# Kernel tuning notes

Measured on AMD Instinct MI355X. Metric: run time of the kernel, lower is better.

## Reference

```python
import jax, jax.numpy as jnp
import numpy as np

E = 4
K = 2
BN_EPS = 1e-3


def _silu(y):
    return y * jax.nn.sigmoid(y)


def _bn_silu_nchw(y, g, b, m, v):
    # eval-mode BatchNorm2d over channel axis of [B, C, H, W], then SiLU
    scale = (g / jnp.sqrt(v + BN_EPS))[None, :, None, None]
    shift = (b - m * g / jnp.sqrt(v + BN_EPS))[None, :, None, None]
    return _silu(y * scale + shift)


def setup_inputs() -> dict:
    key = jax.random.key(0)
    ks = jax.random.split(key, 20)
    B, C1, C2, H, W = 32, 256, 256, 80, 80
    c_ = C2 // 2  # 128
    s = 0.05
    return {
        "x": jax.random.normal(ks[0], (B, C1, H, W), jnp.float32),
        "w1": jax.random.normal(ks[1], (c_, C1), jnp.float32) * s,
        "bn1_g": jax.random.uniform(ks[2], (c_,), jnp.float32, 0.5, 1.5),
        "bn1_b": jax.random.normal(ks[3], (c_,), jnp.float32) * s,
        "bn1_m": jax.random.normal(ks[4], (c_,), jnp.float32) * s,
        "bn1_v": jax.random.uniform(ks[5], (c_,), jnp.float32, 0.5, 1.5),
        "router_w": jax.random.normal(ks[6], (E, c_), jnp.float32) * s,
        "router_b": jax.random.normal(ks[7], (E,), jnp.float32) * s,
        "ew": jax.random.normal(ks[8], (E, c_, c_, 3, 3), jnp.float32) * s,
        "ebn_g": jax.random.uniform(ks[9], (E, c_), jnp.float32, 0.5, 1.5),
        "ebn_b": jax.random.normal(ks[10], (E, c_), jnp.float32) * s,
        "ebn_m": jax.random.normal(ks[11], (E, c_), jnp.float32) * s,
        "ebn_v": jax.random.uniform(ks[12], (E, c_), jnp.float32, 0.5, 1.5),
        "w3": jax.random.normal(ks[13], (C2, c_), jnp.float32) * s,
        "bn3_g": jax.random.uniform(ks[14], (C2,), jnp.float32, 0.5, 1.5),
        "bn3_b": jax.random.normal(ks[15], (C2,), jnp.float32) * s,
        "bn3_m": jax.random.normal(ks[16], (C2,), jnp.float32) * s,
        "bn3_v": jax.random.uniform(ks[17], (C2,), jnp.float32, 0.5, 1.5),
    }


def reference(x, w1, bn1_g, bn1_b, bn1_m, bn1_v, router_w, router_b,
              ew, ebn_g, ebn_b, ebn_m, ebn_v, w3, bn3_g, bn3_b, bn3_m, bn3_v):
    B, C1, H, W = x.shape
    c_ = w1.shape[0]

    # conv1: 1x1 conv + BN + SiLU -> [B, c_, H, W]
    x_in = _bn_silu_nchw(jnp.einsum('bchw,oc->bohw', x, w1), bn1_g, bn1_b, bn1_m, bn1_v)

    # flatten pixels to tokens [N, c_] (N = B*H*W), matching permute(0,2,3,1).reshape
    tokens = x_in.transpose(0, 2, 3, 1).reshape(-1, c_)
    N = tokens.shape[0]

    # router: 1x1 conv with bias -> per-token logits [N, E]
    logits = tokens @ router_w.T + router_b
    probs = jax.nn.softmax(logits, axis=-1)

    topw, topi = jax.lax.top_k(probs, K)                  # [N, K]
    topw = topw / jnp.sum(topw, axis=-1, keepdims=True)

    # dense [N, E] combine weights: normalized top-k weight where selected, else 0
    wd = jnp.zeros((N, E), tokens.dtype).at[jnp.arange(N)[:, None], topi].set(topw)

    # experts: 3x3 conv applied to 1x1 patches with pad=1 -> only center tap matters
    center = ew[:, :, :, 1, 1]                            # [E, c_out, c_in]
    ye = jnp.einsum('nc,eoc->neo', tokens, center)        # [N, E, c_]
    inv = ebn_g / jnp.sqrt(ebn_v + BN_EPS)                # [E, c_]
    ye = _silu(ye * inv[None] + (ebn_b - ebn_m * inv)[None])

    out_moe = jnp.einsum('neo,ne->no', ye, wd)            # weighted scatter-add
    out_moe = out_moe.reshape(B, H, W, c_).transpose(0, 3, 1, 2)

    # conv3: 1x1 conv + BN + SiLU -> [B, C2, H, W]
    x_out = _bn_silu_nchw(jnp.einsum('bchw,oc->bohw', out_moe, w3), bn3_g, bn3_b, bn3_m, bn3_v)

    # shortcut (c1 == c2 here)
    return x_out + x
```

## Files before the change

kernel.cpp:

```cpp
#include <hip/hip_runtime.h>
#include <cstdint>
#include <cstddef>

#define NEXP 4
#define CH   128
#define C1   256
#define C2   256
#define HWSZ 6400
#define NTOKS 204800
#define BNE  1e-3f

using f32x4 = __attribute__((ext_vector_type(4))) float;
using f16x8 = __attribute__((ext_vector_type(8))) _Float16;
using s16x8 = __attribute__((ext_vector_type(8))) short;

static __device__ __forceinline__ unsigned short f2bf(float f) {
    union { float f; unsigned u; } v; v.f = f;
    unsigned r = v.u + 0x7fffu + ((v.u >> 16) & 1u);
    return (unsigned short)(r >> 16);
}
static __device__ __forceinline__ f32x4 zero4() {
    f32x4 z; z[0] = 0.f; z[1] = 0.f; z[2] = 0.f; z[3] = 0.f; return z;
}
static __device__ __forceinline__ void g2lds16(const void* g, void* l) {
    __builtin_amdgcn_global_load_lds(
        (const __attribute__((address_space(1))) void*)g,
        (__attribute__((address_space(3))) void*)l, 16, 0, 0);
}

#define ASWZ(row) ((((row) >> 1) & 3) << 3)

__global__ __launch_bounds__(256) void k0_pack(const float* __restrict__ ew,
                                               const float* __restrict__ w1,
                                               const float* __restrict__ w3,
                                               unsigned short* __restrict__ cen,
                                               _Float16* __restrict__ w1s,
                                               unsigned short* __restrict__ w3p) {
    int bid = blockIdx.x;
    int tid = threadIdx.x;
    if (bid < 256) {
        int idx = bid * 256 + tid;
        cen[idx] = f2bf(ew[(size_t)idx * 9 + 4]);
    } else if (bid < 384) {
        int lin = (bid - 256) * 256 + tid;
        int o = lin >> 8, k = lin & 255;
        int s = k >> 5, kk = k & 31;
        int kks = kk ^ ASWZ(o);
        float v = w1[o * C1 + k];
        _Float16 h = (_Float16)v;
        w1s[((s * 2 + 0) * 128 + o) * 32 + kks] = h;
        w1s[((s * 2 + 1) * 128 + o) * 32 + kks] = (_Float16)((v - (float)h) * 2048.0f);
    } else {
        int lin = (bid - 384) * 256 + tid;
        int o = lin >> 7, k = lin & 127;
        int s = k >> 5, kk = k & 31;
        int kks = kk ^ ASWZ(o);
        w3p[(s * 256 + o) * 32 + kks] = f2bf(w3[o * CH + k]);
    }
}

__global__ __launch_bounds__(256, 2) void k1_conv1_router(
    const float* __restrict__ x, const _Float16* __restrict__ w1s,
    const float* __restrict__ bn1_g, const float* __restrict__ bn1_b,
    const float* __restrict__ bn1_m, const float* __restrict__ bn1_v,
    const float* __restrict__ rw, const float* __restrict__ rb,
    unsigned short* __restrict__ tokens, float* __restrict__ wd)
{
    const int tid  = threadIdx.x;
    const int lane = tid & 63;
    const int n15  = lane & 15;
    const int quad = lane >> 4;
    const int wv   = tid >> 6;

    const int nt0 = blockIdx.x * 64;
    const int b   = nt0 / HWSZ;
    const int hw0 = nt0 % HWSZ;

    __shared__ union {
        struct { _Float16 Ahl[2 * 128 * 32];
                 _Float16 Bh[64 * 40]; _Float16 Bl[64 * 40]; } s;
        struct { float tok[64 * 132]; float logit[64 * 4]; } e;
    } u;
    __shared__ float s1_l[128], t1_l[128];

    if (tid < 128) {
        float s = bn1_g[tid] / sqrtf(bn1_v[tid] + BNE);
        s1_l[tid] = s;
        t1_l[tid] = bn1_b[tid] - bn1_m[tid] * s;
    }

    f32x4 acc_m[2][4], acc_c[2][4];
    #pragma unroll
    for (int i = 0; i < 2; i++)
        #pragma unroll
        for (int j = 0; j < 4; j++) { acc_m[i][j] = zero4(); acc_c[i][j] = zero4(); }

    const char* w1b = (const char*)w1s;
    char*       Ab  = (char*)u.s.Ahl;

    for (int s = 0; s < 8; s++) {
        {
            const char* src = w1b + s * 16384 + tid * 16;
            char*       dst = Ab + tid * 16;
            g2lds16(src + 0,     dst + 0);
            g2lds16(src + 4096,  dst + 4096);
            g2lds16(src + 8192,  dst + 8192);
            g2lds16(src + 12288, dst + 12288);
        }
        {
            int i  = tid & 63;
            int kg = tid >> 6;
            #pragma unroll
            for (int r = 0; r < 2; r++) {
                int k4 = (kg * 2 + r) * 4;
                const float* xp = x + ((size_t)(b * C1 + s * 32 + k4)) * HWSZ + hw0 + i;
                float v0 = xp[0], v1 = xp[HWSZ], v2 = xp[2 * HWSZ], v3 = xp[3 * HWSZ];
                _Float16* bh = &u.s.Bh[i * 40 + k4];
                _Float16* bl = &u.s.Bl[i * 40 + k4];
                _Float16 h0 = (_Float16)v0, h1 = (_Float16)v1, h2 = (_Float16)v2, h3 = (_Float16)v3;
                bh[0] = h0; bh[1] = h1; bh[2] = h2; bh[3] = h3;
                bl[0] = (_Float16)((v0 - (float)h0) * 2048.0f);
                bl[1] = (_Float16)((v1 - (float)h1) * 2048.0f);
                bl[2] = (_Float16)((v2 - (float)h2) * 2048.0f);
                bl[3] = (_Float16)((v3 - (float)h3) * 2048.0f);
            }
        }
        __syncthreads();

        f16x8 a_h[2], a_l[2];
        #pragma unroll
        for (int mt = 0; mt < 2; mt++) {
            int row = (wv * 2 + mt) * 16 + n15;
            int col = (quad * 8) ^ ASWZ(row);
            a_h[mt] = *(const f16x8*)&u.s.Ahl[row * 32 + col];
            a_l[mt] = *(const f16x8*)&u.s.Ahl[4096 + row * 32 + col];
        }
        #pragma unroll
        for (int nt = 0; nt < 4; nt++) {
            int row = nt * 16 + n15;
            f16x8 b_h = *(const f16x8*)&u.s.Bh[row * 40 + quad * 8];
            f16x8 b_l = *(const f16x8*)&u.s.Bl[row * 40 + quad * 8];
            #pragma unroll
            for (int mt = 0; mt < 2; mt++) {
                acc_m[mt][nt] = __builtin_amdgcn_mfma_f32_16x16x32_f16(a_h[mt], b_h, acc_m[mt][nt], 0, 0, 0);
                acc_c[mt][nt] = __builtin_amdgcn_mfma_f32_16x16x32_f16(a_l[mt], b_h, acc_c[mt][nt], 0, 0, 0);
                acc_c[mt][nt] = __builtin_amdgcn_mfma_f32_16x16x32_f16(a_h[mt], b_l, acc_c[mt][nt], 0, 0, 0);
            }
        }
        __syncthreads();
    }

    #pragma unroll
    for (int mt = 0; mt < 2; mt++)
        #pragma unroll
        for (int nt = 0; nt < 4; nt++)
            #pragma unroll
            for (int r = 0; r < 4; r++) {
                int o  = (wv * 2 + mt) * 16 + quad * 4 + r;
                int tk = nt * 16 + n15;
                float y1 = acc_m[mt][nt][r] + acc_c[mt][nt][r] * (1.0f / 2048.0f);
                float y  = y1 * s1_l[o] + t1_l[o];
                u.e.tok[tk * 132 + o] = y / (1.0f + expf(-y));
            }
    __syncthreads();

    {
        int tk = tid >> 2;
        int e  = tid & 3;
        const float* trow = &u.e.tok[tk * 132];
        const float* wrow = &rw[e * CH];
        float a0 = 0.f, a1 = 0.f, a2 = 0.f, a3 = 0.f;
        #pragma unroll 8
        for (int c = 0; c < CH; c += 4) {
            a0 = fmaf(trow[c + 0], wrow[c + 0], a0);
            a1 = fmaf(trow[c + 1], wrow[c + 1], a1);
            a2 = fmaf(trow[c + 2], wrow[c + 2], a2);
            a3 = fmaf(trow[c + 3], wrow[c + 3], a3);
        }
        u.e.logit[tk * 4 + e] = ((a0 + a1) + (a2 + a3)) + rb[e];
    }
    __syncthreads();

    if (tid < 64) {
        const float* lg = &u.e.logit[tid * 4];
        float l0 = lg[0], l1 = lg[1], l2 = lg[2], l3 = lg[3];
        int i1 = 0; float m1 = l0;
        if (l1 > m1) { m1 = l1; i1 = 1; }
        if (l2 > m1) { m1 = l2; i1 = 2; }
        if (l3 > m1) { m1 = l3; i1 = 3; }
        int i2 = -1; float m2 = -3.4e38f;
        if (i1 != 0 && l0 > m2) { m2 = l0; i2 = 0; }
        if (i1 != 1 && l1 > m2) { m2 = l1; i2 = 1; }
        if (i1 != 2 && l2 > m2) { m2 = l2; i2 = 2; }
        if (i1 != 3 && l3 > m2) { m2 = l3; i2 = 3; }
        float p2 = expf(m2 - m1);
        float wa = 1.0f / (1.0f + p2);
        float wb = p2 * wa;
        float4 wout;
        wout.x = (i1 == 0) ? wa : ((i2 == 0) ? wb : 0.0f);
        wout.y = (i1 == 1) ? wa : ((i2 == 1) ? wb : 0.0f);
        wout.z = (i1 == 2) ? wa : ((i2 == 2) ? wb : 0.0f);
        wout.w = (i1 == 3) ? wa : ((i2 == 3) ? wb : 0.0f);
        *(float4*)&wd[(size_t)(nt0 + tid) * 4] = wout;
    }

    #pragma unroll
    for (int rep = 0; rep < 8; rep++) {
        int lin = rep * 256 + tid;
        int n   = lin >> 5;
        int c4  = (lin & 31) * 4;
        const float* tp = &u.e.tok[n * 132 + c4];
        ushort4 pk;
        pk.x = f2bf(tp[0]); pk.y = f2bf(tp[1]); pk.z = f2bf(tp[2]); pk.w = f2bf(tp[3]);
        *(ushort4*)&tokens[(size_t)(nt0 + n) * CH + c4] = pk;
    }
}

__global__ __launch_bounds__(256, 2) void k2_experts(
    const unsigned short* __restrict__ tokens, const unsigned short* __restrict__ cen,
    const float* __restrict__ wd,
    const float* __restrict__ ebn_g, const float* __restrict__ ebn_b,
    const float* __restrict__ ebn_m, const float* __restrict__ ebn_v,
    unsigned short* __restrict__ moe)
{
    const int tid  = threadIdx.x;
    const int lane = tid & 63;
    const int wv   = tid >> 6;
    const int n15  = lane & 15;
    const int quad = lane >> 4;
    const int qm   = wv & 1;
    const int qn   = wv >> 1;
    const int nt0  = blockIdx.x * 128;

    __shared__ unsigned short Bt[128 * 136];
    __shared__ unsigned short Ac[128 * 136];
    __shared__ float wd_l[512];
    __shared__ float inv_l[512], sh_l[512];

    #pragma unroll
    for (int rep = 0; rep < 8; rep++) {
        int lin = rep * 256 + tid;
        int n   = lin >> 4;
        int c8  = (lin & 15) * 8;
        *(uint4*)&Bt[n * 136 + c8] = *(const uint4*)&tokens[(size_t)(nt0 + n) * CH + c8];
    }
    wd_l[tid]       = wd[(size_t)nt0 * 4 + tid];
    wd_l[256 + tid] = wd[(size_t)nt0 * 4 + 256 + tid];
    #pragma unroll
    for (int r = 0; r < 2; r++) {
        int idx = r * 256 + tid;
        float iv = ebn_g[idx] / sqrtf(ebn_v[idx] + BNE);
        inv_l[idx] = iv;
        sh_l[idx]  = ebn_b[idx] - ebn_m[idx] * iv;
    }

    f32x4 oacc[4][4];
    #pragma unroll
    for (int i = 0; i < 4; i++)
        #pragma unroll
        for (int j = 0; j < 4; j++) oacc[i][j] = zero4();

    for (int e = 0; e < NEXP; e++) {
        __syncthreads();
        #pragma unroll
        for (int rep = 0; rep < 8; rep++) {
            int lin = rep * 256 + tid;
            int o   = lin >> 4;
            int c8  = (lin & 15) * 8;
            *(uint4*)&Ac[o * 136 + c8] = *(const uint4*)&cen[(size_t)e * CH * CH + o * CH + c8];
        }
        __syncthreads();

        f32x4 acc[4][4];
        #pragma unroll
        for (int i = 0; i < 4; i++)
            #pragma unroll
            for (int j = 0; j < 4; j++) acc[i][j] = zero4();

        #pragma unroll
        for (int kk = 0; kk < 4; kk++) {
            int ko = kk * 32 + quad * 8;
            s16x8 a[4], bb[4];
            #pragma unroll
            for (int i = 0; i < 4; i++) {
                a[i]  = *(const s16x8*)&Ac[(qm * 64 + i * 16 + n15) * 136 + ko];
                bb[i] = *(const s16x8*)&Bt[(qn * 64 + i * 16 + n15) * 136 + ko];
            }
            #pragma unroll
            for (int mt = 0; mt < 4; mt++)
                #pragma unroll
                for (int nt = 0; nt < 4; nt++)
                    acc[mt][nt] = __builtin_amdgcn_mfma_f32_16x16x32_bf16(a[mt], bb[nt], acc[mt][nt], 0, 0, 0);
        }

        #pragma unroll
        for (int mt = 0; mt < 4; mt++)
            #pragma unroll
            for (int nt = 0; nt < 4; nt++) {
                float wde = wd_l[(qn * 64 + nt * 16 + n15) * 4 + e];
                #pragma unroll
                for (int r = 0; r < 4; r++) {
                    int o = qm * 64 + mt * 16 + quad * 4 + r;
                    float y = acc[mt][nt][r] * inv_l[e * CH + o] + sh_l[e * CH + o];
                    oacc[mt][nt][r] += wde * (y / (1.0f + __expf(-y)));
                }
            }
    }

    #pragma unroll
    for (int mt = 0; mt < 4; mt++)
        #pragma unroll
        for (int nt = 0; nt < 4; nt++) {
            int tk = qn * 64 + nt * 16 + n15;
            int ob = qm * 64 + mt * 16 + quad * 4;
            ushort4 pk;
            pk.x = f2bf(oacc[mt][nt][0]); pk.y = f2bf(oacc[mt][nt][1]);
            pk.z = f2bf(oacc[mt][nt][2]); pk.w = f2bf(oacc[mt][nt][3]);
            *(ushort4*)&moe[(size_t)(nt0 + tk) * CH + ob] = pk;
        }
}

__global__ __launch_bounds__(256, 2) void k3_conv3(
    const unsigned short* __restrict__ moe, const unsigned short* __restrict__ w3p,
    const float* __restrict__ bn3_g, const float* __restrict__ bn3_b,
    const float* __restrict__ bn3_m, const float* __restrict__ bn3_v,
    const float* __restrict__ x, float* __restrict__ out)
{
    const int tid  = threadIdx.x;
    const int lane = tid & 63;
    const int wv   = tid >> 6;
    const int n15  = lane & 15;
    const int quad = lane >> 4;
    const int nt0  = blockIdx.x * 64;
    const int b    = nt0 / HWSZ;
    const int hw0  = nt0 % HWSZ;

    __shared__ unsigned short A3[256 * 32];
    __shared__ unsigned short B3[64 * 40];
    __shared__ float s3_l[256], t3_l[256];

    {
        float s = bn3_g[tid] / sqrtf(bn3_v[tid] + BNE);
        s3_l[tid] = s;
        t3_l[tid] = bn3_b[tid] - bn3_m[tid] * s;
    }

    f32x4 acc[4][4];
    #pragma unroll
    for (int i = 0; i < 4; i++)
        #pragma unroll
        for (int j = 0; j < 4; j++) acc[i][j] = zero4();

    const char* w3b = (const char*)w3p;
    char*       Ab  = (char*)A3;

    for (int s = 0; s < 4; s++) {
        {
            const char* src = w3b + s * 16384 + tid * 16;
            char*       dst = Ab + tid * 16;
            g2lds16(src + 0,     dst + 0);
            g2lds16(src + 4096,  dst + 4096);
            g2lds16(src + 8192,  dst + 8192);
            g2lds16(src + 12288, dst + 12288);
        }
        #pragma unroll
        for (int rep = 0; rep < 2; rep++) {
            int lin = rep * 256 + tid;
            int n   = lin >> 3;
            int k4  = (lin & 7) * 4;
            *(ushort4*)&B3[n * 40 + k4] = *(const ushort4*)&moe[(size_t)(nt0 + n) * CH + s * 32 + k4];
        }
        __syncthreads();

        s16x8 bf[4];
        #pragma unroll
        for (int nt = 0; nt < 4; nt++)
            bf[nt] = *(const s16x8*)&B3[(nt * 16 + n15) * 40 + quad * 8];
        #pragma unroll
        for (int mt = 0; mt < 4; mt++) {
            int row = (wv * 4 + mt) * 16 + n15;
            int col = (quad * 8) ^ ASWZ(row);
            s16x8 af = *(const s16x8*)&A3[row * 32 + col];
            #pragma unroll
            for (int nt = 0; nt < 4; nt++)
                acc[mt][nt] = __builtin_amdgcn_mfma_f32_16x16x32_bf16(af, bf[nt], acc[mt][nt], 0, 0, 0);
        }
        __syncthreads();
    }

    #pragma unroll
    for (int mt = 0; mt < 4; mt++)
        #pragma unroll
        for (int nt = 0; nt < 4; nt++)
            #pragma unroll
            for (int r = 0; r < 4; r++) {
                int o2 = (wv * 4 + mt) * 16 + quad * 4 + r;
                int tk = nt * 16 + n15;
                size_t g = ((size_t)(b * C2 + o2)) * HWSZ + hw0 + tk;
                float y = acc[mt][nt][r] * s3_l[o2] + t3_l[o2];
                out[g] = y / (1.0f + __expf(-y)) + x[g];
            }
}

extern "C" void kernel_launch(void* const* d_in, const int* in_sizes, int n_in,
                              void* d_out, int out_size, void* d_ws, size_t ws_size,
                              hipStream_t stream) {
    const float* x     = (const float*)d_in[0];
    const float* w1    = (const float*)d_in[1];
    const float* bn1_g = (const float*)d_in[2];
    const float* bn1_b = (const float*)d_in[3];
    const float* bn1_m = (const float*)d_in[4];
    const float* bn1_v = (const float*)d_in[5];
    const float* rw    = (const float*)d_in[6];
    const float* rb    = (const float*)d_in[7];
    const float* ew    = (const float*)d_in[8];
    const float* ebn_g = (const float*)d_in[9];
    const float* ebn_b = (const float*)d_in[10];
    const float* ebn_m = (const float*)d_in[11];
    const float* ebn_v = (const float*)d_in[12];
    const float* w3    = (const float*)d_in[13];
    const float* bn3_g = (const float*)d_in[14];
    const float* bn3_b = (const float*)d_in[15];
    const float* bn3_m = (const float*)d_in[16];
    const float* bn3_v = (const float*)d_in[17];
    float* out = (float*)d_out;

    char* ws = (char*)d_ws;
    unsigned short* tokens = (unsigned short*)(ws);
    unsigned short* moe    = (unsigned short*)(ws + 52428800);
    float*          wdv    = (float*)(ws + 104857600);
    unsigned short* cen    = (unsigned short*)(ws + 108134400);
    _Float16*       w1s    = (_Float16*)(ws + 108265472);
    unsigned short* w3p    = (unsigned short*)(ws + 108396544);

    k0_pack<<<dim3(512), dim3(256), 0, stream>>>(ew, w1, w3, cen, w1s, w3p);
    k1_conv1_router<<<dim3(3200), dim3(256), 0, stream>>>(x, w1s, bn1_g, bn1_b, bn1_m, bn1_v,
                                                          rw, rb, tokens, wdv);
    k2_experts<<<dim3(1600), dim3(256), 0, stream>>>(tokens, cen, wdv,
                                                     ebn_g, ebn_b, ebn_m, ebn_v, moe);
    k3_conv3<<<dim3(3200), dim3(256), 0, stream>>>(moe, w3p, bn3_g, bn3_b, bn3_m, bn3_v, x, out);
    (void)in_sizes; (void)n_in; (void)out_size; (void)ws_size;
}
```

Before: 630.6 us.

## Fuse expert MoE and conv3 kernels, keep MoE tile in LDS

Merges the expert kernel and the conv3 kernel into one. The bf16 MoE output tile stays in shared memory and is reused as the B operand for conv3, which removes the write and re-read of the 52 MB intermediate through HBM. The conv3 epilogue is staged through LDS so the output and residual accesses use coalesced float4 along the pixel axis, and k1 swaps expf for __expf. In exchange, conv3 now processes 128 tokens per block with a 4x8 accumulator array, which raises register pressure and may lower occupancy.

```diff
diff --git a/kernel.cpp b/kernel.cpp
--- a/kernel.cpp
+++ b/kernel.cpp
@@ -160,7 +160,7 @@
                 int tk = nt * 16 + n15;
                 float y1 = acc_m[mt][nt][r] + acc_c[mt][nt][r] * (1.0f / 2048.0f);
                 float y  = y1 * s1_l[o] + t1_l[o];
-                u.e.tok[tk * 132 + o] = y / (1.0f + expf(-y));
+                u.e.tok[tk * 132 + o] = y / (1.0f + __expf(-y));
             }
     __syncthreads();
 
@@ -193,7 +193,7 @@
         if (i1 != 1 && l1 > m2) { m2 = l1; i2 = 1; }
         if (i1 != 2 && l2 > m2) { m2 = l2; i2 = 2; }
         if (i1 != 3 && l3 > m2) { m2 = l3; i2 = 3; }
-        float p2 = expf(m2 - m1);
+        float p2 = __expf(m2 - m1);
         float wa = 1.0f / (1.0f + p2);
         float wb = p2 * wa;
         float4 wout;
@@ -216,12 +216,14 @@
     }
 }
 
-__global__ __launch_bounds__(256, 2) void k2_experts(
+__global__ __launch_bounds__(256, 2) void k23_experts_conv3(
     const unsigned short* __restrict__ tokens, const unsigned short* __restrict__ cen,
-    const float* __restrict__ wd,
+    const float* __restrict__ wd, const unsigned short* __restrict__ w3p,
     const float* __restrict__ ebn_g, const float* __restrict__ ebn_b,
     const float* __restrict__ ebn_m, const float* __restrict__ ebn_v,
-    unsigned short* __restrict__ moe)
+    const float* __restrict__ bn3_g, const float* __restrict__ bn3_b,
+    const float* __restrict__ bn3_m, const float* __restrict__ bn3_v,
+    const float* __restrict__ x, float* __restrict__ out)
 {
     const int tid  = threadIdx.x;
     const int lane = tid & 63;
@@ -231,18 +233,23 @@
     const int qm   = wv & 1;
     const int qn   = wv >> 1;
     const int nt0  = blockIdx.x * 128;
-
-    __shared__ unsigned short Bt[128 * 136];
-    __shared__ unsigned short Ac[128 * 136];
+    const int b    = nt0 / HWSZ;
+    const int hw0  = nt0 % HWSZ;
+
+    __shared__ union {
+        struct { unsigned short Bt[128 * 136]; unsigned short Ac[128 * 136]; } p;
+        float scr[128 * 132];
+    } u;
     __shared__ float wd_l[512];
     __shared__ float inv_l[512], sh_l[512];
+    __shared__ float s3_l[256], t3_l[256];
 
     #pragma unroll
     for (int rep = 0; rep < 8; rep++) {
         int lin = rep * 256 + tid;
         int n   = lin >> 4;
         int c8  = (lin & 15) * 8;
-        *(uint4*)&Bt[n * 136 + c8] = *(const uint4*)&tokens[(size_t)(nt0 + n) * CH + c8];
+        *(uint4*)&u.p.Bt[n * 136 + c8] = *(const uint4*)&tokens[(size_t)(nt0 + n) * CH + c8];
     }
     wd_l[tid]       = wd[(size_t)nt0 * 4 + tid];
     wd_l[256 + tid] = wd[(size_t)nt0 * 4 + 256 + tid];
@@ -253,6 +260,11 @@
         inv_l[idx] = iv;
         sh_l[idx]  = ebn_b[idx] - ebn_m[idx] * iv;
     }
+    {
+        float s = bn3_g[tid] / sqrtf(bn3_v[tid] + BNE);
+        s3_l[tid] = s;
+        t3_l[tid] = bn3_b[tid] - bn3_m[tid] * s;
+    }
 
     f32x4 oacc[4][4];
     #pragma unroll
@@ -267,7 +279,7 @@
             int lin = rep * 256 + tid;
             int o   = lin >> 4;
             int c8  = (lin & 15) * 8;
-            *(uint4*)&Ac[o * 136 + c8] = *(const uint4*)&cen[(size_t)e * CH * CH + o * CH + c8];
+            *(uint4*)&u.p.Ac[o * 136 + c8] = *(const uint4*)&cen[(size_t)e * CH * CH + o * CH + c8];
         }
         __syncthreads();
 
@@ -283,8 +295,8 @@
             s16x8 a[4], bb[4];
             #pragma unroll
             for (int i = 0; i < 4; i++) {
-                a[i]  = *(const s16x8*)&Ac[(qm * 64 + i * 16 + n15) * 136 + ko];
-                bb[i] = *(const s16x8*)&Bt[(qn * 64 + i * 16 + n15) * 136 + ko];
+                a[i]  = *(const s16x8*)&u.p.Ac[(qm * 64 + i * 16 + n15) * 136 + ko];
+                bb[i] = *(const s16x8*)&u.p.Bt[(qn * 64 + i * 16 + n15) * 136 + ko];
             }
             #pragma unroll
             for (int mt = 0; mt < 4; mt++)
@@ -307,6 +319,7 @@
             }
     }
 
+    __syncthreads();
     #pragma unroll
     for (int mt = 0; mt < 4; mt++)
         #pragma unroll
@@ -316,45 +329,20 @@
             ushort4 pk;
             pk.x = f2bf(oacc[mt][nt][0]); pk.y = f2bf(oacc[mt][nt][1]);
             pk.z = f2bf(oacc[mt][nt][2]); pk.w = f2bf(oacc[mt][nt][3]);
-            *(ushort4*)&moe[(size_t)(nt0 + tk) * CH + ob] = pk;
-        }
-}
-
-__global__ __launch_bounds__(256, 2) void k3_conv3(
-    const unsigned short* __restrict__ moe, const unsigned short* __restrict__ w3p,
-    const float* __restrict__ bn3_g, const float* __restrict__ bn3_b,
-    const float* __restrict__ bn3_m, const float* __restrict__ bn3_v,
-    const float* __restrict__ x, float* __restrict__ out)
-{
-    const int tid  = threadIdx.x;
-    const int lane = tid & 63;
-    const int wv   = tid >> 6;
-    const int n15  = lane & 15;
-    const int quad = lane >> 4;
-    const int nt0  = blockIdx.x * 64;
-    const int b    = nt0 / HWSZ;
-    const int hw0  = nt0 % HWSZ;
-
-    __shared__ unsigned short A3[256 * 32];
-    __shared__ unsigned short B3[64 * 40];
-    __shared__ float s3_l[256], t3_l[256];
-
-    {
-        float s = bn3_g[tid] / sqrtf(bn3_v[tid] + BNE);
-        s3_l[tid] = s;
-        t3_l[tid] = bn3_b[tid] - bn3_m[tid] * s;
-    }
-
-    f32x4 acc[4][4];
+            *(ushort4*)&u.p.Bt[tk * 136 + ob] = pk;
+        }
+
+    f32x4 acc3[4][8];
     #pragma unroll
     for (int i = 0; i < 4; i++)
         #pragma unroll
-        for (int j = 0; j < 4; j++) acc[i][j] = zero4();
+        for (int j = 0; j < 8; j++) acc3[i][j] = zero4();
 
     const char* w3b = (const char*)w3p;
-    char*       Ab  = (char*)A3;
+    char*       Ab  = (char*)u.p.Ac;
 
     for (int s = 0; s < 4; s++) {
+        __syncthreads();
         {
             const char* src = w3b + s * 16384 + tid * 16;
             char*       dst = Ab + tid * 16;
@@ -363,43 +351,57 @@
             g2lds16(src + 8192,  dst + 8192);
             g2lds16(src + 12288, dst + 12288);
         }
-        #pragma unroll
-        for (int rep = 0; rep < 2; rep++) {
-            int lin = rep * 256 + tid;
-            int n   = lin >> 3;
-            int k4  = (lin & 7) * 4;
-            *(ushort4*)&B3[n * 40 + k4] = *(const ushort4*)&moe[(size_t)(nt0 + n) * CH + s * 32 + k4];
-        }
-        __syncthreads();
-
-        s16x8 bf[4];
-        #pragma unroll
-        for (int nt = 0; nt < 4; nt++)
-            bf[nt] = *(const s16x8*)&B3[(nt * 16 + n15) * 40 + quad * 8];
+        __syncthreads();
+
+        s16x8 bf[8];
+        #pragma unroll
+        for (int nt = 0; nt < 8; nt++)
+            bf[nt] = *(const s16x8*)&u.p.Bt[(nt * 16 + n15) * 136 + s * 32 + quad * 8];
         #pragma unroll
         for (int mt = 0; mt < 4; mt++) {
             int row = (wv * 4 + mt) * 16 + n15;
             int col = (quad * 8) ^ ASWZ(row);
-            s16x8 af = *(const s16x8*)&A3[row * 32 + col];
-            #pragma unroll
-            for (int nt = 0; nt < 4; nt++)
-                acc[mt][nt] = __builtin_amdgcn_mfma_f32_16x16x32_bf16(af, bf[nt], acc[mt][nt], 0, 0, 0);
-        }
-        __syncthreads();
-    }
-
-    #pragma unroll
-    for (int mt = 0; mt < 4; mt++)
-        #pragma unroll
-        for (int nt = 0; nt < 4; nt++)
-            #pragma unroll
-            for (int r = 0; r < 4; r++) {
-                int o2 = (wv * 4 + mt) * 16 + quad * 4 + r;
-                int tk = nt * 16 + n15;
-                size_t g = ((size_t)(b * C2 + o2)) * HWSZ + hw0 + tk;
-                float y = acc[mt][nt][r] * s3_l[o2] + t3_l[o2];
-                out[g] = y / (1.0f + __expf(-y)) + x[g];
-            }
+            s16x8 af = *(const s16x8*)&u.p.Ac[row * 32 + col];
+            #pragma unroll
+            for (int nt = 0; nt < 8; nt++)
+                acc3[mt][nt] = __builtin_amdgcn_mfma_f32_16x16x32_bf16(af, bf[nt], acc3[mt][nt], 0, 0, 0);
+        }
+    }
+
+    #pragma unroll
+    for (int h = 0; h < 2; h++) {
+        __syncthreads();
+        if ((wv >> 1) == h) {
+            int wvl = wv & 1;
+            #pragma unroll
+            for (int mt = 0; mt < 4; mt++)
+                #pragma unroll
+                for (int nt = 0; nt < 8; nt++) {
+                    int tk = nt * 16 + n15;
+                    #pragma unroll
+                    for (int r = 0; r < 4; r++) {
+                        int o_l = wvl * 64 + mt * 16 + quad * 4 + r;
+                        int o2  = h * 128 + o_l;
+                        float y = acc3[mt][nt][r] * s3_l[o2] + t3_l[o2];
+                        u.scr[o_l * 132 + tk] = y / (1.0f + __expf(-y));
+                    }
+                }
+        }
+        __syncthreads();
+        #pragma unroll
+        for (int rep = 0; rep < 16; rep++) {
+            int lin = rep * 256 + tid;
+            int o_l = lin >> 5;
+            int tk4 = (lin & 31) * 4;
+            int o2  = h * 128 + o_l;
+            size_t g = ((size_t)(b * C2 + o2)) * HWSZ + hw0 + tk4;
+            f32x4 v = *(const f32x4*)&u.scr[o_l * 132 + tk4];
+            const float4 xs = *(const float4*)&x[g];
+            float4 w;
+            w.x = v[0] + xs.x; w.y = v[1] + xs.y; w.z = v[2] + xs.z; w.w = v[3] + xs.w;
+            *(float4*)&out[g] = w;
+        }
+    }
 }
 
 extern "C" void kernel_launch(void* const* d_in, const int* in_sizes, int n_in,
@@ -427,7 +429,6 @@
 
     char* ws = (char*)d_ws;
     unsigned short* tokens = (unsigned short*)(ws);
-    unsigned short* moe    = (unsigned short*)(ws + 52428800);
     float*          wdv    = (float*)(ws + 104857600);
     unsigned short* cen    = (unsigned short*)(ws + 108134400);
     _Float16*       w1s    = (_Float16*)(ws + 108265472);
@@ -436,8 +437,8 @@
     k0_pack<<<dim3(512), dim3(256), 0, stream>>>(ew, w1, w3, cen, w1s, w3p);
     k1_conv1_router<<<dim3(3200), dim3(256), 0, stream>>>(x, w1s, bn1_g, bn1_b, bn1_m, bn1_v,
                                                           rw, rb, tokens, wdv);
-    k2_experts<<<dim3(1600), dim3(256), 0, stream>>>(tokens, cen, wdv,
-                                                     ebn_g, ebn_b, ebn_m, ebn_v, moe);
-    k3_conv3<<<dim3(3200), dim3(256), 0, stream>>>(moe, w3p, bn3_g, bn3_b, bn3_m, bn3_v, x, out);
+    k23_experts_conv3<<<dim3(1600), dim3(256), 0, stream>>>(tokens, cen, wdv, w3p,
+                                                            ebn_g, ebn_b, ebn_m, ebn_v,
+                                                            bn3_g, bn3_b, bn3_m, bn3_v, x, out);
     (void)in_sizes; (void)n_in; (void)out_size; (void)ws_size;
 }
```

Result: slower. 664.1 us (+5.3%).

## Load weights directly from global into registers and vectorize conv3 epilogue stores

Applied to the files above, without the earlier changes.

Weight tiles in conv1, the expert GEMM and conv3 are now read straight from global memory into registers instead of being staged through LDS, which frees shared memory and removes barriers. Conv1 handles 64 input channels per stage with half as many syncs, and occupancy hints go up for conv1 and conv3. Conv3 loads its whole activation tile once, then transposes outputs through an LDS scratch buffer so the residual add and stores use coalesced float4 accesses. expf is replaced by __expf. The tradeoffs are more redundant global and cache reads of weights across waves and higher register pressure.

```diff
diff --git a/kernel.cpp b/kernel.cpp
--- a/kernel.cpp
+++ b/kernel.cpp
@@ -21,11 +21,6 @@
 }
 static __device__ __forceinline__ f32x4 zero4() {
     f32x4 z; z[0] = 0.f; z[1] = 0.f; z[2] = 0.f; z[3] = 0.f; return z;
-}
-static __device__ __forceinline__ void g2lds16(const void* g, void* l) {
-    __builtin_amdgcn_global_load_lds(
-        (const __attribute__((address_space(1))) void*)g,
-        (__attribute__((address_space(3))) void*)l, 16, 0, 0);
 }
 
 #define ASWZ(row) ((((row) >> 1) & 3) << 3)
@@ -59,7 +54,7 @@
     }
 }
 
-__global__ __launch_bounds__(256, 2) void k1_conv1_router(
+__global__ __launch_bounds__(256, 4) void k1_conv1_router(
     const float* __restrict__ x, const _Float16* __restrict__ w1s,
     const float* __restrict__ bn1_g, const float* __restrict__ bn1_b,
     const float* __restrict__ bn1_m, const float* __restrict__ bn1_v,
@@ -77,8 +72,7 @@
     const int hw0 = nt0 % HWSZ;
 
     __shared__ union {
-        struct { _Float16 Ahl[2 * 128 * 32];
-                 _Float16 Bh[64 * 40]; _Float16 Bl[64 * 40]; } s;
+        struct { _Float16 Bh[64 * 72]; _Float16 Bl[64 * 72]; } s;
         struct { float tok[64 * 132]; float logit[64 * 4]; } e;
     } u;
     __shared__ float s1_l[128], t1_l[128];
@@ -95,28 +89,17 @@
         #pragma unroll
         for (int j = 0; j < 4; j++) { acc_m[i][j] = zero4(); acc_c[i][j] = zero4(); }
 
-    const char* w1b = (const char*)w1s;
-    char*       Ab  = (char*)u.s.Ahl;
-
-    for (int s = 0; s < 8; s++) {
-        {
-            const char* src = w1b + s * 16384 + tid * 16;
-            char*       dst = Ab + tid * 16;
-            g2lds16(src + 0,     dst + 0);
-            g2lds16(src + 4096,  dst + 4096);
-            g2lds16(src + 8192,  dst + 8192);
-            g2lds16(src + 12288, dst + 12288);
-        }
+    for (int S = 0; S < 4; S++) {
         {
             int i  = tid & 63;
             int kg = tid >> 6;
             #pragma unroll
-            for (int r = 0; r < 2; r++) {
-                int k4 = (kg * 2 + r) * 4;
-                const float* xp = x + ((size_t)(b * C1 + s * 32 + k4)) * HWSZ + hw0 + i;
+            for (int r = 0; r < 4; r++) {
+                int k4 = kg * 16 + r * 4;
+                const float* xp = x + ((size_t)(b * C1 + S * 64 + k4)) * HWSZ + hw0 + i;
                 float v0 = xp[0], v1 = xp[HWSZ], v2 = xp[2 * HWSZ], v3 = xp[3 * HWSZ];
-                _Float16* bh = &u.s.Bh[i * 40 + k4];
-                _Float16* bl = &u.s.Bl[i * 40 + k4];
+                _Float16* bh = &u.s.Bh[i * 72 + k4];
+                _Float16* bl = &u.s.Bl[i * 72 + k4];
                 _Float16 h0 = (_Float16)v0, h1 = (_Float16)v1, h2 = (_Float16)v2, h3 = (_Float16)v3;
                 bh[0] = h0; bh[1] = h1; bh[2] = h2; bh[3] = h3;
                 bl[0] = (_Float16)((v0 - (float)h0) * 2048.0f);
@@ -127,24 +110,28 @@
         }
         __syncthreads();
 
-        f16x8 a_h[2], a_l[2];
-        #pragma unroll
-        for (int mt = 0; mt < 2; mt++) {
-            int row = (wv * 2 + mt) * 16 + n15;
-            int col = (quad * 8) ^ ASWZ(row);
-            a_h[mt] = *(const f16x8*)&u.s.Ahl[row * 32 + col];
-            a_l[mt] = *(const f16x8*)&u.s.Ahl[4096 + row * 32 + col];
-        }
-        #pragma unroll
-        for (int nt = 0; nt < 4; nt++) {
-            int row = nt * 16 + n15;
-            f16x8 b_h = *(const f16x8*)&u.s.Bh[row * 40 + quad * 8];
-            f16x8 b_l = *(const f16x8*)&u.s.Bl[row * 40 + quad * 8];
+        #pragma unroll
+        for (int kh = 0; kh < 2; kh++) {
+            const int sl = S * 2 + kh;
+            f16x8 a_h[2], a_l[2];
             #pragma unroll
             for (int mt = 0; mt < 2; mt++) {
-                acc_m[mt][nt] = __builtin_amdgcn_mfma_f32_16x16x32_f16(a_h[mt], b_h, acc_m[mt][nt], 0, 0, 0);
-                acc_c[mt][nt] = __builtin_amdgcn_mfma_f32_16x16x32_f16(a_l[mt], b_h, acc_c[mt][nt], 0, 0, 0);
-                acc_c[mt][nt] = __builtin_amdgcn_mfma_f32_16x16x32_f16(a_h[mt], b_l, acc_c[mt][nt], 0, 0, 0);
+                int row = (wv * 2 + mt) * 16 + n15;
+                int col = (quad * 8) ^ ASWZ(row);
+                a_h[mt] = *(const f16x8*)&w1s[((sl * 2 + 0) * 128 + row) * 32 + col];
+                a_l[mt] = *(const f16x8*)&w1s[((sl * 2 + 1) * 128 + row) * 32 + col];
+            }
+            #pragma unroll
+            for (int nt = 0; nt < 4; nt++) {
+                int row = nt * 16 + n15;
+                f16x8 b_h = *(const f16x8*)&u.s.Bh[row * 72 + kh * 32 + quad * 8];
+                f16x8 b_l = *(const f16x8*)&u.s.Bl[row * 72 + kh * 32 + quad * 8];
+                #pragma unroll
+                for (int mt = 0; mt < 2; mt++) {
+                    acc_m[mt][nt] = __builtin_amdgcn_mfma_f32_16x16x32_f16(a_h[mt], b_h, acc_m[mt][nt], 0, 0, 0);
+                    acc_c[mt][nt] = __builtin_amdgcn_mfma_f32_16x16x32_f16(a_l[mt], b_h, acc_c[mt][nt], 0, 0, 0);
+                    acc_c[mt][nt] = __builtin_amdgcn_mfma_f32_16x16x32_f16(a_h[mt], b_l, acc_c[mt][nt], 0, 0, 0);
+                }
             }
         }
         __syncthreads();
@@ -160,7 +147,7 @@
                 int tk = nt * 16 + n15;
                 float y1 = acc_m[mt][nt][r] + acc_c[mt][nt][r] * (1.0f / 2048.0f);
                 float y  = y1 * s1_l[o] + t1_l[o];
-                u.e.tok[tk * 132 + o] = y / (1.0f + expf(-y));
+                u.e.tok[tk * 132 + o] = y / (1.0f + __expf(-y));
             }
     __syncthreads();
 
@@ -193,7 +180,7 @@
         if (i1 != 1 && l1 > m2) { m2 = l1; i2 = 1; }
         if (i1 != 2 && l2 > m2) { m2 = l2; i2 = 2; }
         if (i1 != 3 && l3 > m2) { m2 = l3; i2 = 3; }
-        float p2 = expf(m2 - m1);
+        float p2 = __expf(m2 - m1);
         float wa = 1.0f / (1.0f + p2);
         float wb = p2 * wa;
         float4 wout;
@@ -233,7 +220,6 @@
     const int nt0  = blockIdx.x * 128;
 
     __shared__ unsigned short Bt[128 * 136];
-    __shared__ unsigned short Ac[128 * 136];
     __shared__ float wd_l[512];
     __shared__ float inv_l[512], sh_l[512];
 
@@ -260,16 +246,15 @@
         #pragma unroll
         for (int j = 0; j < 4; j++) oacc[i][j] = zero4();
 
+    __syncthreads();
+
     for (int e = 0; e < NEXP; e++) {
-        __syncthreads();
-        #pragma unroll
-        for (int rep = 0; rep < 8; rep++) {
-            int lin = rep * 256 + tid;
-            int o   = lin >> 4;
-            int c8  = (lin & 15) * 8;
-            *(uint4*)&Ac[o * 136 + c8] = *(const uint4*)&cen[(size_t)e * CH * CH + o * CH + c8];
-        }
-        __syncthreads();
+        s16x8 a[4][4];
+        #pragma unroll
+        for (int kk = 0; kk < 4; kk++)
+            #pragma unroll
+            for (int i = 0; i < 4; i++)
+                a[kk][i] = *(const s16x8*)&cen[((size_t)e * CH + qm * 64 + i * 16 + n15) * CH + kk * 32 + quad * 8];
 
         f32x4 acc[4][4];
         #pragma unroll
@@ -280,17 +265,15 @@
         #pragma unroll
         for (int kk = 0; kk < 4; kk++) {
             int ko = kk * 32 + quad * 8;
-            s16x8 a[4], bb[4];
-            #pragma unroll
-            for (int i = 0; i < 4; i++) {
-                a[i]  = *(const s16x8*)&Ac[(qm * 64 + i * 16 + n15) * 136 + ko];
+            s16x8 bb[4];
+            #pragma unroll
+            for (int i = 0; i < 4; i++)
                 bb[i] = *(const s16x8*)&Bt[(qn * 64 + i * 16 + n15) * 136 + ko];
-            }
             #pragma unroll
             for (int mt = 0; mt < 4; mt++)
                 #pragma unroll
                 for (int nt = 0; nt < 4; nt++)
-                    acc[mt][nt] = __builtin_amdgcn_mfma_f32_16x16x32_bf16(a[mt], bb[nt], acc[mt][nt], 0, 0, 0);
+                    acc[mt][nt] = __builtin_amdgcn_mfma_f32_16x16x32_bf16(a[kk][mt], bb[nt], acc[mt][nt], 0, 0, 0);
         }
 
         #pragma unroll
@@ -320,7 +303,7 @@
         }
 }
 
-__global__ __launch_bounds__(256, 2) void k3_conv3(
+__global__ __launch_bounds__(256, 3) void k3_conv3(
     const unsigned short* __restrict__ moe, const unsigned short* __restrict__ w3p,
     const float* __restrict__ bn3_g, const float* __restrict__ bn3_b,
     const float* __restrict__ bn3_m, const float* __restrict__ bn3_v,
@@ -335,8 +318,10 @@
     const int b    = nt0 / HWSZ;
     const int hw0  = nt0 % HWSZ;
 
-    __shared__ unsigned short A3[256 * 32];
-    __shared__ unsigned short B3[64 * 40];
+    __shared__ union {
+        unsigned short B3[64 * 136];
+        float scr[128 * 68];
+    } u;
     __shared__ float s3_l[256], t3_l[256];
 
     {
@@ -345,61 +330,76 @@
         t3_l[tid] = bn3_b[tid] - bn3_m[tid] * s;
     }
 
+    #pragma unroll
+    for (int rep = 0; rep < 2; rep++) {
+        int lin = rep * 256 + tid;
+        int n   = lin >> 3;
+        int c16 = (lin & 7) * 16;
+        *(uint4*)&u.B3[n * 136 + c16]     = *(const uint4*)&moe[(size_t)(nt0 + n) * CH + c16];
+        *(uint4*)&u.B3[n * 136 + c16 + 8] = *(const uint4*)&moe[(size_t)(nt0 + n) * CH + c16 + 8];
+    }
+
     f32x4 acc[4][4];
     #pragma unroll
     for (int i = 0; i < 4; i++)
         #pragma unroll
         for (int j = 0; j < 4; j++) acc[i][j] = zero4();
 
-    const char* w3b = (const char*)w3p;
-    char*       Ab  = (char*)A3;
+    __syncthreads();
 
     for (int s = 0; s < 4; s++) {
-        {
-            const char* src = w3b + s * 16384 + tid * 16;
-            char*       dst = Ab + tid * 16;
-            g2lds16(src + 0,     dst + 0);
-            g2lds16(src + 4096,  dst + 4096);
-            g2lds16(src + 8192,  dst + 8192);
-            g2lds16(src + 12288, dst + 12288);
-        }
-        #pragma unroll
-        for (int rep = 0; rep < 2; rep++) {
-            int lin = rep * 256 + tid;
-            int n   = lin >> 3;
-            int k4  = (lin & 7) * 4;
-            *(ushort4*)&B3[n * 40 + k4] = *(const ushort4*)&moe[(size_t)(nt0 + n) * CH + s * 32 + k4];
-        }
-        __syncthreads();
-
-        s16x8 bf[4];
-        #pragma unroll
-        for (int nt = 0; nt < 4; nt++)
-            bf[nt] = *(const s16x8*)&B3[(nt * 16 + n15) * 40 + quad * 8];
+        s16x8 af[4];
         #pragma unroll
         for (int mt = 0; mt < 4; mt++) {
             int row = (wv * 4 + mt) * 16 + n15;
             int col = (quad * 8) ^ ASWZ(row);
-            s16x8 af = *(const s16x8*)&A3[row * 32 + col];
+            af[mt] = *(const s16x8*)&w3p[(s * 256 + row) * 32 + col];
+        }
+        s16x8 bf[4];
+        #pragma unroll
+        for (int nt = 0; nt < 4; nt++)
+            bf[nt] = *(const s16x8*)&u.B3[(nt * 16 + n15) * 136 + s * 32 + quad * 8];
+        #pragma unroll
+        for (int mt = 0; mt < 4; mt++)
             #pragma unroll
             for (int nt = 0; nt < 4; nt++)
-                acc[mt][nt] = __builtin_amdgcn_mfma_f32_16x16x32_bf16(af, bf[nt], acc[mt][nt], 0, 0, 0);
-        }
+                acc[mt][nt] = __builtin_amdgcn_mfma_f32_16x16x32_bf16(af[mt], bf[nt], acc[mt][nt], 0, 0, 0);
+    }
+
+    #pragma unroll
+    for (int h = 0; h < 2; h++) {
         __syncthreads();
-    }
-
-    #pragma unroll
-    for (int mt = 0; mt < 4; mt++)
-        #pragma unroll
-        for (int nt = 0; nt < 4; nt++)
-            #pragma unroll
-            for (int r = 0; r < 4; r++) {
-                int o2 = (wv * 4 + mt) * 16 + quad * 4 + r;
-                int tk = nt * 16 + n15;
-                size_t g = ((size_t)(b * C2 + o2)) * HWSZ + hw0 + tk;
-                float y = acc[mt][nt][r] * s3_l[o2] + t3_l[o2];
-                out[g] = y / (1.0f + __expf(-y)) + x[g];
-            }
+        if ((wv >> 1) == h) {
+            int wvl = wv & 1;
+            #pragma unroll
+            for (int mt = 0; mt < 4; mt++)
+                #pragma unroll
+                for (int nt = 0; nt < 4; nt++) {
+                    int tk = nt * 16 + n15;
+                    #pragma unroll
+                    for (int r = 0; r < 4; r++) {
+                        int o_l = wvl * 64 + mt * 16 + quad * 4 + r;
+                        int o2  = h * 128 + o_l;
+                        float y = acc[mt][nt][r] * s3_l[o2] + t3_l[o2];
+                        u.scr[o_l * 68 + tk] = y / (1.0f + __expf(-y));
+                    }
+                }
+        }
+        __syncthreads();
+        #pragma unroll
+        for (int rep = 0; rep < 8; rep++) {
+            int lin = rep * 256 + tid;
+            int row = lin >> 4;
+            int t4  = (lin & 15) * 4;
+            int o2  = h * 128 + row;
+            size_t g = ((size_t)(b * C2 + o2)) * HWSZ + hw0 + t4;
+            f32x4 v = *(const f32x4*)&u.scr[row * 68 + t4];
+            const float4 xs = *(const float4*)&x[g];
+            float4 w;
+            w.x = v[0] + xs.x; w.y = v[1] + xs.y; w.z = v[2] + xs.z; w.w = v[3] + xs.w;
+            *(float4*)&out[g] = w;
+        }
+    }
 }
 
 extern "C" void kernel_launch(void* const* d_in, const int* in_sizes, int n_in,
```

After: 654.3 us. 3.8% more time.
